# Optimization experiments

Measured on AMD Instinct MI355X. Metric: run time of the kernel, lower is better.

The kernel has to match this reference:

```python
import jax, jax.numpy as jnp
import numpy as np


def setup_inputs() -> dict:
    key = jax.random.key(0)
    ks = jax.random.split(key, 6)
    B, T, D, U = 32, 2048, 512, 512
    scale = 1.0 / np.sqrt(D)
    return {
        "values": jax.random.normal(ks[0], (B, T, D), dtype=jnp.float32),
        "query": jax.random.normal(ks[1], (B, D), dtype=jnp.float32),
        "W1": jax.random.normal(ks[2], (D, U), dtype=jnp.float32) * scale,
        "b1": jnp.zeros((U,), dtype=jnp.float32),
        "W2": jax.random.normal(ks[3], (D, U), dtype=jnp.float32) * scale,
        "b2": jnp.zeros((U,), dtype=jnp.float32),
        "V": jax.random.normal(ks[4], (U, 1), dtype=jnp.float32) * (1.0 / np.sqrt(U)),
        "bV": jnp.zeros((1,), dtype=jnp.float32),
    }


def reference(values, query, W1, b1, W2, b2, V, bV):
    # values: [B,T,D], query: [B,D]
    proj_v = jnp.einsum("btd,du->btu", values, W1) + b1          # [B,T,U]
    proj_q = (query @ W2 + b2)[:, None, :]                        # [B,1,U]
    score = jnp.tanh(proj_v + proj_q) @ V + bV                    # [B,T,1]
    attention_weights = jax.nn.softmax(score, axis=1)             # [B,T,1]
    context_vector = jnp.sum(attention_weights * values, axis=1)  # [B,D]
    return context_vector, attention_weights
```

## Files before the change

### kernel.cpp

```cpp
#include <hip/hip_runtime.h>
#include <math.h>


#define B_ 32
#define T_ 2048
#define D_ 512
#define U_ 512
#define M_ (B_ * T_)

typedef _Float16 half8 __attribute__((ext_vector_type(8)));
typedef float floatx4 __attribute__((ext_vector_type(4)));

__global__ __launch_bounds__(256) void projq_kernel(
    const float* __restrict__ query, const float* __restrict__ W2,
    const float* __restrict__ b2, float* __restrict__ projq) {
  const int b = blockIdx.x;
  const int u = blockIdx.y * 256 + threadIdx.x;
  __shared__ float q[D_];
  for (int d = threadIdx.x; d < D_; d += 256) q[d] = query[b * D_ + d];
  __syncthreads();
  float acc = 0.f;
#pragma unroll 8
  for (int d = 0; d < D_; ++d) acc += q[d] * W2[d * U_ + u];
  projq[b * U_ + u] = acc + b2[u];
}

__global__ __launch_bounds__(256) void score_mfma_kernel(
    const float* __restrict__ values, const float* __restrict__ W1,
    const float* __restrict__ b1, const float* __restrict__ projq,
    const float* __restrict__ V, float* __restrict__ scores) {
  const int m0 = blockIdx.x * 128;
  const int u0 = blockIdx.y * 128;
  const int b = blockIdx.x >> 4;
  const int tid = threadIdx.x;

  __shared__ alignas(16) _Float16 As[128 * 32];
  __shared__ alignas(16) _Float16 Bs[128 * 32];

  const int lane = tid & 63;
  const int w = tid >> 6;
  const int wm = (w & 1) * 64;
  const int wn = (w >> 1) * 64;
  const int ln = lane & 15;
  const int lq = lane >> 4;

  floatx4 acc[4][4] = {};

  const int srow = tid >> 1;
  const int skoff = (tid & 1) * 16;
  const float* aptr = values + (long)(m0 + srow) * D_ + skoff;
  const float* bptr = W1 + u0 + srow;

  for (int k0 = 0; k0 < D_; k0 += 32) {
    const float4 a0 = *(const float4*)(aptr + k0);
    const float4 a1 = *(const float4*)(aptr + k0 + 4);
    const float4 a2 = *(const float4*)(aptr + k0 + 8);
    const float4 a3 = *(const float4*)(aptr + k0 + 12);
    half8 ha0 = {(_Float16)a0.x, (_Float16)a0.y, (_Float16)a0.z, (_Float16)a0.w,
                 (_Float16)a1.x, (_Float16)a1.y, (_Float16)a1.z, (_Float16)a1.w};
    half8 ha1 = {(_Float16)a2.x, (_Float16)a2.y, (_Float16)a2.z, (_Float16)a2.w,
                 (_Float16)a3.x, (_Float16)a3.y, (_Float16)a3.z, (_Float16)a3.w};
    float bt[16];
#pragma unroll
    for (int kk = 0; kk < 16; ++kk)
      bt[kk] = bptr[(long)(k0 + skoff + kk) * U_];
    half8 hb0 = {(_Float16)bt[0], (_Float16)bt[1], (_Float16)bt[2], (_Float16)bt[3],
                 (_Float16)bt[4], (_Float16)bt[5], (_Float16)bt[6], (_Float16)bt[7]};
    half8 hb1 = {(_Float16)bt[8], (_Float16)bt[9], (_Float16)bt[10], (_Float16)bt[11],
                 (_Float16)bt[12], (_Float16)bt[13], (_Float16)bt[14], (_Float16)bt[15]};

    *(half8*)&As[srow * 32 + skoff] = ha0;
    *(half8*)&As[srow * 32 + skoff + 8] = ha1;
    *(half8*)&Bs[srow * 32 + skoff] = hb0;
    *(half8*)&Bs[srow * 32 + skoff + 8] = hb1;
    __syncthreads();

    half8 af[4], bf[4];
#pragma unroll
    for (int i = 0; i < 4; ++i) {
      af[i] = *(const half8*)&As[(wm + i * 16 + ln) * 32 + lq * 8];
      bf[i] = *(const half8*)&Bs[(wn + i * 16 + ln) * 32 + lq * 8];
    }
#pragma unroll
    for (int mi = 0; mi < 4; ++mi)
#pragma unroll
      for (int ni = 0; ni < 4; ++ni)
        acc[mi][ni] = __builtin_amdgcn_mfma_f32_16x16x32_f16(
            af[mi], bf[ni], acc[mi][ni], 0, 0, 0);
    __syncthreads();
  }

  float pre[4], vv[4];
#pragma unroll
  for (int ni = 0; ni < 4; ++ni) {
    const int u = u0 + wn + ni * 16 + ln;
    pre[ni] = b1[u] + projq[b * U_ + u];
    vv[ni] = V[u];
  }
#pragma unroll
  for (int mi = 0; mi < 4; ++mi) {
#pragma unroll
    for (int r = 0; r < 4; ++r) {
      float t = 0.f;
#pragma unroll
      for (int ni = 0; ni < 4; ++ni)
        t += tanhf(acc[mi][ni][r] + pre[ni]) * vv[ni];
      t += __shfl_xor(t, 1);
      t += __shfl_xor(t, 2);
      t += __shfl_xor(t, 4);
      t += __shfl_xor(t, 8);
      if (ln == mi * 4 + r)
        atomicAdd(scores + m0 + wm + mi * 16 + lq * 4 + r, t);
    }
  }
}

__global__ __launch_bounds__(256) void softmax_kernel(
    const float* __restrict__ scores, float* __restrict__ weights) {
  const int b = blockIdx.x;
  const int tid = threadIdx.x;
  float v[8];
  float mx = -INFINITY;
#pragma unroll
  for (int i = 0; i < 8; ++i) {
    v[i] = scores[b * T_ + i * 256 + tid];
    mx = fmaxf(mx, v[i]);
  }
#pragma unroll
  for (int off = 32; off > 0; off >>= 1) mx = fmaxf(mx, __shfl_down(mx, off));
  __shared__ float sm[4], ss[4];
  if ((tid & 63) == 0) sm[tid >> 6] = mx;
  __syncthreads();
  mx = fmaxf(fmaxf(sm[0], sm[1]), fmaxf(sm[2], sm[3]));
  float sum = 0.f;
#pragma unroll
  for (int i = 0; i < 8; ++i) {
    v[i] = __expf(v[i] - mx);
    sum += v[i];
  }
#pragma unroll
  for (int off = 32; off > 0; off >>= 1) sum += __shfl_down(sum, off);
  if ((tid & 63) == 0) ss[tid >> 6] = sum;
  __syncthreads();
  const float inv = 1.f / (ss[0] + ss[1] + ss[2] + ss[3]);
#pragma unroll
  for (int i = 0; i < 8; ++i) weights[b * T_ + i * 256 + tid] = v[i] * inv;
}

__global__ __launch_bounds__(256) void context_kernel(
    const float* __restrict__ values, const float* __restrict__ weights,
    float* __restrict__ context) {
  const int b = blockIdx.x;
  const int t0 = blockIdx.y * 64;
  const int tid = threadIdx.x;
  __shared__ float w[64];
  if (tid < 64) w[tid] = weights[b * T_ + t0 + tid];
  __syncthreads();
  float2 acc = make_float2(0.f, 0.f);
  const float2* vp = (const float2*)(values + (long)(b * T_ + t0) * D_) + tid;
#pragma unroll 4
  for (int t = 0; t < 64; ++t) {
    const float2 x = vp[(long)t * (D_ / 2)];
    acc.x += w[t] * x.x;
    acc.y += w[t] * x.y;
  }
  atomicAdd(context + b * D_ + tid * 2 + 0, acc.x);
  atomicAdd(context + b * D_ + tid * 2 + 1, acc.y);
}

extern "C" void kernel_launch(void* const* d_in, const int* in_sizes, int n_in,
                              void* d_out, int out_size, void* d_ws, size_t ws_size,
                              hipStream_t stream) {
  const float* values = (const float*)d_in[0];
  const float* query = (const float*)d_in[1];
  const float* W1 = (const float*)d_in[2];
  const float* b1 = (const float*)d_in[3];
  const float* W2 = (const float*)d_in[4];
  const float* b2 = (const float*)d_in[5];
  const float* V = (const float*)d_in[6];

  float* out = (float*)d_out;
  float* context = out;
  float* weights = out + B_ * D_;
  float* projq = (float*)d_ws;
  float* scores = projq + B_ * U_;

  hipMemsetAsync(scores, 0, M_ * sizeof(float), stream);
  hipMemsetAsync(context, 0, B_ * D_ * sizeof(float), stream);

  projq_kernel<<<dim3(B_, U_ / 256), 256, 0, stream>>>(query, W2, b2, projq);
  score_mfma_kernel<<<dim3(M_ / 128, U_ / 128), 256, 0, stream>>>(
      values, W1, b1, projq, V, scores);
  softmax_kernel<<<B_, 256, 0, stream>>>(scores, weights);
  context_kernel<<<dim3(B_, T_ / 64), 256, 0, stream>>>(values, weights, context);
}
```

Before: 361.0 us.

## Restructure score GEMM to full-U rows with pre-transposed fp16 W1

The W1 matrix is transposed and converted to fp16 once per call in a new prep kernel. The score kernel now has each block own 32 rows across all 512 U columns, with the values tile resident in LDS and B fragments read straight from global memory. Per-row scores are reduced in shared memory and stored directly, which removes the atomics and both memsets; zeroing of the context output moves into the softmax kernel. The change also swaps tanhf for an exp-based fast tanh and uses float4 loads with a two-group reduction in the context kernel. The risks are higher register pressure from 16 accumulators and uncached global B fragment loads.

```diff
diff --git a/kernel.cpp b/kernel.cpp
--- a/kernel.cpp
+++ b/kernel.cpp
@@ -7,9 +7,16 @@
 #define D_ 512
 #define U_ 512
 #define M_ (B_ * T_)
+#define ASTRIDE 520
 
 typedef _Float16 half8 __attribute__((ext_vector_type(8)));
 typedef float floatx4 __attribute__((ext_vector_type(4)));
+
+__device__ __forceinline__ float fast_tanh(float x) {
+  x = fminf(fmaxf(x, -20.f), 20.f);
+  const float e = __expf(2.f * x);
+  return 1.f - 2.f / (e + 1.f);
+}
 
 __global__ __launch_bounds__(256) void projq_kernel(
     const float* __restrict__ query, const float* __restrict__ W2,
@@ -25,98 +32,114 @@
   projq[b * U_ + u] = acc + b2[u];
 }
 
-__global__ __launch_bounds__(256) void score_mfma_kernel(
-    const float* __restrict__ values, const float* __restrict__ W1,
+__global__ __launch_bounds__(256) void prep_w1t(
+    const float* __restrict__ W1, _Float16* __restrict__ w1t) {
+  __shared__ float t[64][65];
+  const int k0 = blockIdx.x * 64, u0 = blockIdx.y * 64;
+  const int lu = threadIdx.x & 63;
+  const int g = threadIdx.x >> 6;
+#pragma unroll
+  for (int i = 0; i < 16; ++i) {
+    const int row = g * 16 + i;
+    t[row][lu] = W1[(long)(k0 + row) * U_ + u0 + lu];
+  }
+  __syncthreads();
+#pragma unroll
+  for (int i = 0; i < 16; ++i) {
+    const int row = g * 16 + i;
+    w1t[(long)(u0 + row) * D_ + k0 + lu] = (_Float16)t[lu][row];
+  }
+}
+
+__global__ __launch_bounds__(256) void score_fused_kernel(
+    const float* __restrict__ values, const _Float16* __restrict__ w1t,
     const float* __restrict__ b1, const float* __restrict__ projq,
     const float* __restrict__ V, float* __restrict__ scores) {
-  const int m0 = blockIdx.x * 128;
-  const int u0 = blockIdx.y * 128;
-  const int b = blockIdx.x >> 4;
+  const int m0 = blockIdx.x * 32;
+  const int b = blockIdx.x >> 6;
   const int tid = threadIdx.x;
-
-  __shared__ alignas(16) _Float16 As[128 * 32];
-  __shared__ alignas(16) _Float16 Bs[128 * 32];
-
   const int lane = tid & 63;
   const int w = tid >> 6;
-  const int wm = (w & 1) * 64;
-  const int wn = (w >> 1) * 64;
+  const int wn = w * 128;
   const int ln = lane & 15;
   const int lq = lane >> 4;
 
-  floatx4 acc[4][4] = {};
-
-  const int srow = tid >> 1;
-  const int skoff = (tid & 1) * 16;
-  const float* aptr = values + (long)(m0 + srow) * D_ + skoff;
-  const float* bptr = W1 + u0 + srow;
+  __shared__ alignas(16) _Float16 As[32 * ASTRIDE];
+  __shared__ float red[4][32];
+
+  {
+    const float* vbase = values + (long)m0 * D_;
+#pragma unroll
+    for (int it = 0; it < 16; ++it) {
+      const int f = it * 256 + tid;
+      const int row = f >> 7;
+      const int kk = (f & 127) * 4;
+      const float4 v = *(const float4*)(vbase + (long)row * D_ + kk);
+      _Float16* p = &As[row * ASTRIDE + kk];
+      p[0] = (_Float16)v.x;
+      p[1] = (_Float16)v.y;
+      p[2] = (_Float16)v.z;
+      p[3] = (_Float16)v.w;
+    }
+  }
+  __syncthreads();
+
+  const _Float16* bp[8];
+#pragma unroll
+  for (int ni = 0; ni < 8; ++ni)
+    bp[ni] = w1t + (long)(wn + ni * 16 + ln) * D_ + lq * 8;
+
+  floatx4 acc[2][8] = {};
 
   for (int k0 = 0; k0 < D_; k0 += 32) {
-    const float4 a0 = *(const float4*)(aptr + k0);
-    const float4 a1 = *(const float4*)(aptr + k0 + 4);
-    const float4 a2 = *(const float4*)(aptr + k0 + 8);
-    const float4 a3 = *(const float4*)(aptr + k0 + 12);
-    half8 ha0 = {(_Float16)a0.x, (_Float16)a0.y, (_Float16)a0.z, (_Float16)a0.w,
-                 (_Float16)a1.x, (_Float16)a1.y, (_Float16)a1.z, (_Float16)a1.w};
-    half8 ha1 = {(_Float16)a2.x, (_Float16)a2.y, (_Float16)a2.z, (_Float16)a2.w,
-                 (_Float16)a3.x, (_Float16)a3.y, (_Float16)a3.z, (_Float16)a3.w};
-    float bt[16];
-#pragma unroll
-    for (int kk = 0; kk < 16; ++kk)
-      bt[kk] = bptr[(long)(k0 + skoff + kk) * U_];
-    half8 hb0 = {(_Float16)bt[0], (_Float16)bt[1], (_Float16)bt[2], (_Float16)bt[3],
-                 (_Float16)bt[4], (_Float16)bt[5], (_Float16)bt[6], (_Float16)bt[7]};
-    half8 hb1 = {(_Float16)bt[8], (_Float16)bt[9], (_Float16)bt[10], (_Float16)bt[11],
-                 (_Float16)bt[12], (_Float16)bt[13], (_Float16)bt[14], (_Float16)bt[15]};
-
-    *(half8*)&As[srow * 32 + skoff] = ha0;
-    *(half8*)&As[srow * 32 + skoff + 8] = ha1;
-    *(half8*)&Bs[srow * 32 + skoff] = hb0;
-    *(half8*)&Bs[srow * 32 + skoff + 8] = hb1;
-    __syncthreads();
-
-    half8 af[4], bf[4];
-#pragma unroll
-    for (int i = 0; i < 4; ++i) {
-      af[i] = *(const half8*)&As[(wm + i * 16 + ln) * 32 + lq * 8];
-      bf[i] = *(const half8*)&Bs[(wn + i * 16 + ln) * 32 + lq * 8];
-    }
-#pragma unroll
-    for (int mi = 0; mi < 4; ++mi)
-#pragma unroll
-      for (int ni = 0; ni < 4; ++ni)
+    half8 af[2];
+#pragma unroll
+    for (int mi = 0; mi < 2; ++mi)
+      af[mi] = *(const half8*)&As[(mi * 16 + ln) * ASTRIDE + k0 + lq * 8];
+    half8 bf[8];
+#pragma unroll
+    for (int ni = 0; ni < 8; ++ni) bf[ni] = *(const half8*)(bp[ni] + k0);
+#pragma unroll
+    for (int mi = 0; mi < 2; ++mi)
+#pragma unroll
+      for (int ni = 0; ni < 8; ++ni)
         acc[mi][ni] = __builtin_amdgcn_mfma_f32_16x16x32_f16(
             af[mi], bf[ni], acc[mi][ni], 0, 0, 0);
-    __syncthreads();
-  }
-
-  float pre[4], vv[4];
-#pragma unroll
-  for (int ni = 0; ni < 4; ++ni) {
-    const int u = u0 + wn + ni * 16 + ln;
+  }
+
+  float pre[8], vv[8];
+#pragma unroll
+  for (int ni = 0; ni < 8; ++ni) {
+    const int u = wn + ni * 16 + ln;
     pre[ni] = b1[u] + projq[b * U_ + u];
     vv[ni] = V[u];
   }
 #pragma unroll
-  for (int mi = 0; mi < 4; ++mi) {
+  for (int mi = 0; mi < 2; ++mi) {
 #pragma unroll
     for (int r = 0; r < 4; ++r) {
       float t = 0.f;
 #pragma unroll
-      for (int ni = 0; ni < 4; ++ni)
-        t += tanhf(acc[mi][ni][r] + pre[ni]) * vv[ni];
+      for (int ni = 0; ni < 8; ++ni)
+        t += fast_tanh(acc[mi][ni][r] + pre[ni]) * vv[ni];
       t += __shfl_xor(t, 1);
       t += __shfl_xor(t, 2);
       t += __shfl_xor(t, 4);
       t += __shfl_xor(t, 8);
-      if (ln == mi * 4 + r)
-        atomicAdd(scores + m0 + wm + mi * 16 + lq * 4 + r, t);
+      if (ln == 0) red[w][mi * 16 + lq * 4 + r] = t;
     }
   }
+  __syncthreads();
+  if (tid < 32)
+    scores[m0 + tid] =
+        red[0][tid] + red[1][tid] + red[2][tid] + red[3][tid];
 }
 
 __global__ __launch_bounds__(256) void softmax_kernel(
-    const float* __restrict__ scores, float* __restrict__ weights) {
+    const float* __restrict__ scores, float* __restrict__ weights,
+    float* __restrict__ context) {
+  ((float2*)context)[blockIdx.x * 256 + threadIdx.x] = make_float2(0.f, 0.f);
+
   const int b = blockIdx.x;
   const int tid = threadIdx.x;
   float v[8];
@@ -153,19 +176,29 @@
   const int b = blockIdx.x;
   const int t0 = blockIdx.y * 64;
   const int tid = threadIdx.x;
-  __shared__ float w[64];
-  if (tid < 64) w[tid] = weights[b * T_ + t0 + tid];
-  __syncthreads();
-  float2 acc = make_float2(0.f, 0.f);
-  const float2* vp = (const float2*)(values + (long)(b * T_ + t0) * D_) + tid;
+  const int g = tid >> 7;
+  const int dx = tid & 127;
+  __shared__ float wsh[64];
+  __shared__ float4 part[128];
+  if (tid < 64) wsh[tid] = weights[b * T_ + t0 + tid];
+  __syncthreads();
+  float4 acc = make_float4(0.f, 0.f, 0.f, 0.f);
+  const float4* vp = (const float4*)(values + (long)(b * T_ + t0 + g) * D_) + dx;
 #pragma unroll 4
-  for (int t = 0; t < 64; ++t) {
-    const float2 x = vp[(long)t * (D_ / 2)];
-    acc.x += w[t] * x.x;
-    acc.y += w[t] * x.y;
-  }
-  atomicAdd(context + b * D_ + tid * 2 + 0, acc.x);
-  atomicAdd(context + b * D_ + tid * 2 + 1, acc.y);
+  for (int t = 0; t < 32; ++t) {
+    const float4 x = vp[(long)(2 * t) * (D_ / 4)];
+    const float ww = wsh[2 * t + g];
+    acc.x += ww * x.x; acc.y += ww * x.y; acc.z += ww * x.z; acc.w += ww * x.w;
+  }
+  if (g == 0) part[dx] = acc;
+  __syncthreads();
+  if (g == 1) {
+    const float4 p = part[dx];
+    atomicAdd(&context[b * D_ + dx * 4 + 0], acc.x + p.x);
+    atomicAdd(&context[b * D_ + dx * 4 + 1], acc.y + p.y);
+    atomicAdd(&context[b * D_ + dx * 4 + 2], acc.z + p.z);
+    atomicAdd(&context[b * D_ + dx * 4 + 3], acc.w + p.w);
+  }
 }
 
 extern "C" void kernel_launch(void* const* d_in, const int* in_sizes, int n_in,
@@ -184,13 +217,12 @@
   float* weights = out + B_ * D_;
   float* projq = (float*)d_ws;
   float* scores = projq + B_ * U_;
-
-  hipMemsetAsync(scores, 0, M_ * sizeof(float), stream);
-  hipMemsetAsync(context, 0, B_ * D_ * sizeof(float), stream);
+  _Float16* w1t = (_Float16*)((char*)d_ws + 65536 + 262144);
 
   projq_kernel<<<dim3(B_, U_ / 256), 256, 0, stream>>>(query, W2, b2, projq);
-  score_mfma_kernel<<<dim3(M_ / 128, U_ / 128), 256, 0, stream>>>(
-      values, W1, b1, projq, V, scores);
-  softmax_kernel<<<B_, 256, 0, stream>>>(scores, weights);
+  prep_w1t<<<dim3(D_ / 64, U_ / 64), 256, 0, stream>>>(W1, w1t);
+  score_fused_kernel<<<M_ / 32, 256, 0, stream>>>(
+      values, w1t, b1, projq, V, scores);
+  softmax_kernel<<<B_, 256, 0, stream>>>(scores, weights, context);
   context_kernel<<<dim3(B_, T_ / 64), 256, 0, stream>>>(values, weights, context);
 }
```

New measurement: 400.0 us. 10.8% more time.
